# Kernel optimization log

Measured on AMD Instinct MI355X. Metric: run time of the kernel, lower is better.

Reference implementation:

```python
import jax, jax.numpy as jnp
import numpy as np

B, N, D, E, A, DIAM = 16, 1024, 128, 16384, 64, 3


def setup_inputs() -> dict:
    key = jax.random.key(0)
    ks = jax.random.split(key, 20)
    s = 0.05
    inp = {
        "node_features": jax.random.normal(ks[0], (B, N, D), jnp.float32),
        "edge_features": jax.random.normal(ks[1], (B, N, N), jnp.float32),
        "src_idx": jax.random.randint(ks[2], (E,), 0, N, jnp.int32),
        "tgt_idx": jax.random.randint(ks[3], (E,), 0, N, jnp.int32),
        # message MLP: Linear(2D+1 -> D)
        "W_msg": jax.random.normal(ks[4], (2 * D + 1, D), jnp.float32) * s,
        "b_msg": jax.random.normal(ks[5], (D,), jnp.float32) * s,
        # GRUCell(D, D), gate order r,z,n (torch convention)
        "W_ih": jax.random.normal(ks[6], (3 * D, D), jnp.float32) * s,
        "W_hh": jax.random.normal(ks[7], (3 * D, D), jnp.float32) * s,
        "b_ih": jax.random.normal(ks[8], (3 * D,), jnp.float32) * s,
        "b_hh": jax.random.normal(ks[9], (3 * D,), jnp.float32) * s,
        # readout: Linear(D,D)+SELU, Linear(D,D)+SELU, then policy head Linear(D,A)
        "W_r1": jax.random.normal(ks[10], (D, D), jnp.float32) * s,
        "b_r1": jax.random.normal(ks[11], (D,), jnp.float32) * s,
        "W_r2": jax.random.normal(ks[12], (D, D), jnp.float32) * s,
        "b_r2": jax.random.normal(ks[13], (D,), jnp.float32) * s,
        "W_pol": jax.random.normal(ks[14], (D, A), jnp.float32) * s,
        "b_pol": jax.random.normal(ks[15], (A,), jnp.float32) * s,
    }
    return inp


def reference(node_features, edge_features, src_idx, tgt_idx,
              W_msg, b_msg, W_ih, W_hh, b_ih, b_hh,
              W_r1, b_r1, W_r2, b_r2, W_pol, b_pol):
    h = node_features  # [B, N, D]
    ef = edge_features[:, src_idx, tgt_idx][..., None]  # [B, E, 1], constant across rounds
    for _ in range(DIAM):
        src_f = h[:, src_idx]  # [B, E, D] gather
        tgt_f = h[:, tgt_idx]  # [B, E, D]
        comb = jnp.concatenate([src_f, tgt_f, ef], axis=-1)  # [B, E, 2D+1]
        msg = jax.nn.selu(comb @ W_msg + b_msg)  # [B, E, D]
        # scatter-sum messages onto target nodes
        agg = jax.vmap(lambda m: jax.ops.segment_sum(m, tgt_idx, num_segments=N))(msg)  # [B, N, D]
        # GRUCell update (torch math, gate order r,z,n; b_hn stays inside r*(...))
        gi = agg @ W_ih.T + b_ih  # [B, N, 3D]
        gh = h @ W_hh.T + b_hh    # [B, N, 3D]
        i_r, i_z, i_n = jnp.split(gi, 3, axis=-1)
        h_r, h_z, h_n = jnp.split(gh, 3, axis=-1)
        r = jax.nn.sigmoid(i_r + h_r)
        z = jax.nn.sigmoid(i_z + h_z)
        n = jnp.tanh(i_n + r * h_n)
        h = (1.0 - z) * n + z * h
    pooled = h.sum(axis=1)  # [B, D]
    pooled = jax.nn.selu(pooled @ W_r1 + b_r1)
    pooled = jax.nn.selu(pooled @ W_r2 + b_r2)
    return pooled @ W_pol + b_pol  # [B, A] policy logits
```

## Files before the change

kernel.cpp:

```cpp
#include <hip/hip_runtime.h>
#include <hip/hip_bf16.h>
#include <math.h>

constexpr int kB = 16;
constexpr int kN = 1024;
constexpr int kD = 128;
constexpr int kE = 16384;

typedef short bf16x8 __attribute__((ext_vector_type(8)));
typedef float f32x4 __attribute__((ext_vector_type(4)));
typedef unsigned short us4 __attribute__((ext_vector_type(4)));

__device__ __forceinline__ float selu_f(float x) {
    const float scale = 1.0507009873554805f;
    const float alpha = 1.6732632423543772f;
    return x > 0.f ? scale * x : scale * alpha * (__expf(x) - 1.f);
}

__device__ __forceinline__ float sigmoid_f(float x) {
    return __builtin_amdgcn_rcpf(1.f + __expf(-x));
}

__device__ __forceinline__ float tanh_f(float x) {
    return 1.f - 2.f * __builtin_amdgcn_rcpf(1.f + __expf(2.f * x));
}

__device__ __forceinline__ float bf2f(unsigned short u) {
    union { unsigned int i; float f; } x;
    x.i = ((unsigned int)u) << 16;
    return x.f;
}

__device__ __forceinline__ unsigned short f2bf(float f) {
    union { float f; unsigned int i; } u;
    u.f = f;
    const unsigned int r = u.i + 0x7fffu + ((u.i >> 16) & 1u);
    return (unsigned short)(r >> 16);
}

__global__ void k_h0cw(const float* __restrict__ nodef, unsigned short* __restrict__ h_bf,
                       const int* __restrict__ tgt, int* __restrict__ cnt,
                       const float* __restrict__ Wmsg, const float* __restrict__ Whh,
                       const float* __restrict__ Wih,
                       const float* __restrict__ bih, const float* __restrict__ bhh,
                       unsigned short* __restrict__ WcatT,
                       unsigned short* __restrict__ Wfused,
                       float* __restrict__ bihP, float* __restrict__ bhhP) {
    const int bid = blockIdx.x;
    const int t = threadIdx.x;
    if (bid < 2048) {
        const int gid = bid * 256 + t;
        const float4 v = ((const float4*)nodef)[gid];
        us4 o;
        o.x = f2bf(v.x);
        o.y = f2bf(v.y);
        o.z = f2bf(v.z);
        o.w = f2bf(v.w);
        ((us4*)h_bf)[gid] = o;
        if (gid < kE) atomicAdd(&cnt[tgt[gid]], 1);
    } else {
        const int j = (bid - 2048) * 2 + (t >> 7);
        const int k = t & 127;
        if (j < 256) {
            float v = (j < 128) ? Wmsg[k * 128 + j] : Wmsg[(128 + k) * 128 + (j - 128)];
            WcatT[j * 128 + k] = f2bf(v);
        } else {
            const int f = j - 256;
            const int dg = f / 48, rem = f % 48;
            const int g = rem / 16, di = rem % 16;
            const int orig = g * 128 + dg * 16 + di;
            Wfused[(size_t)f * 256 + k] = f2bf(Wih[(size_t)orig * 128 + k]);
            Wfused[(size_t)f * 256 + 128 + k] = f2bf(Whh[(size_t)orig * 128 + k]);
            if (k == 0) {
                bihP[f] = bih[orig];
                bhhP[f] = bhh[orig];
            }
        }
    }
}

__launch_bounds__(1024)
__global__ void k_scansct(const int* __restrict__ cnt, const int* __restrict__ src,
                          const int* __restrict__ tgt, int* __restrict__ rowstart,
                          int* __restrict__ ssrc, int* __restrict__ stgt) {
    __shared__ int s[kN];
    __shared__ int cur[kN];
    const int t = threadIdx.x;
    const int own = cnt[t];
    s[t] = own;
    __syncthreads();
    for (int off = 1; off < kN; off <<= 1) {
        int add = (t >= off) ? s[t - off] : 0;
        __syncthreads();
        s[t] += add;
        __syncthreads();
    }
    const int excl = s[t] - own;
    cur[t] = excl;
    rowstart[t] = excl;
    if (t == kN - 1) rowstart[kN] = s[t];
    __syncthreads();
    for (int e = t; e < kE; e += 1024) {
        const int tg = tgt[e];
        const int pos = atomicAdd(&cur[tg], 1);
        ssrc[pos] = src[e];
        stgt[pos] = tg;
    }
}

__global__ void k_gather_ef(const float* __restrict__ edgef, const int* __restrict__ ssrc,
                            const int* __restrict__ stgt, float* __restrict__ efg) {
    const int gid = blockIdx.x * 256 + threadIdx.x;
    const int b = gid >> 14;
    const int i = gid & (kE - 1);
    efg[gid] = edgef[(size_t)b * kN * kN + (size_t)ssrc[i] * kN + stgt[i]];
}

__launch_bounds__(256)
__global__ void k_mm256(const unsigned short* __restrict__ A,
                        const unsigned short* __restrict__ Bt,
                        unsigned short* __restrict__ HST) {
    __shared__ uint4 As[2048];
    __shared__ uint4 Bs[2048];
    const int t = threadIdx.x;
    const int r0 = blockIdx.x * 128;
    const int c0 = blockIdx.y * 128;
    const uint4* gA = (const uint4*)(A + (size_t)r0 * 128);
    const uint4* gB = (const uint4*)(Bt + (size_t)c0 * 128);
#pragma unroll
    for (int i = 0; i < 8; ++i) {
        const int f = i * 256 + t;
        const int row = f >> 4, c16 = f & 15;
        const int d = row * 16 + (c16 ^ (row & 7));
        As[d] = gA[f];
        Bs[d] = gB[f];
    }
    __syncthreads();
    const int w = t >> 6, l = t & 63;
    const int wm = (w & 1) * 64, wn = (w >> 1) * 64;
    const int lin = l & 15, kq = l >> 4;
    f32x4 acc[4][4] = {};
#pragma unroll
    for (int s = 0; s < 4; ++s) {
        bf16x8 a[4], b[4];
#pragma unroll
        for (int mi = 0; mi < 4; ++mi) {
            const int row = wm + mi * 16 + lin;
            a[mi] = *(const bf16x8*)&As[row * 16 + ((s * 4 + kq) ^ (row & 7))];
        }
#pragma unroll
        for (int ni = 0; ni < 4; ++ni) {
            const int row = wn + ni * 16 + lin;
            b[ni] = *(const bf16x8*)&Bs[row * 16 + ((s * 4 + kq) ^ (row & 7))];
        }
#pragma unroll
        for (int mi = 0; mi < 4; ++mi)
#pragma unroll
            for (int ni = 0; ni < 4; ++ni)
                acc[mi][ni] = __builtin_amdgcn_mfma_f32_16x16x32_bf16(
                    b[ni], a[mi], acc[mi][ni], 0, 0, 0);
    }
    const int rq = kq * 4;
#pragma unroll
    for (int mi = 0; mi < 4; ++mi) {
        const int row = r0 + wm + mi * 16 + lin;
#pragma unroll
        for (int ni = 0; ni < 4; ++ni) {
            const int col = c0 + wn + ni * 16 + rq;
            us4 o;
            o.x = f2bf(acc[mi][ni][0]);
            o.y = f2bf(acc[mi][ni][1]);
            o.z = f2bf(acc[mi][ni][2]);
            o.w = f2bf(acc[mi][ni][3]);
            *(us4*)&HST[(size_t)row * 256 + col] = o;
        }
    }
}

__launch_bounds__(256)
__global__ void k_edge(const unsigned short* __restrict__ HST, const float* __restrict__ efg,
                       const int* __restrict__ ssrc, const int* __restrict__ rowstart,
                       const float* __restrict__ Wmsg, const float* __restrict__ bmsg,
                       unsigned short* __restrict__ agg_bf) {
    __shared__ float4 part[2][4][32];
    const int t = threadIdx.x;
    const int b = blockIdx.y;
    const int tl = t >> 7;
    const int tg = blockIdx.x * 2 + tl;
    const int slot = (t >> 5) & 3;
    const int lane = t & 31;
    const int c = lane * 4;
    const float4 w3 = *(const float4*)&Wmsg[256 * 128 + c];
    const float4 bm = *(const float4*)&bmsg[c];
    const size_t base = (size_t)b * kN;
    const us4 htu = *(const us4*)&HST[(base + tg) * 256 + 128 + c];
    const float hb0 = bf2f(htu.x) + bm.x;
    const float hb1 = bf2f(htu.y) + bm.y;
    const float hb2 = bf2f(htu.z) + bm.z;
    const float hb3 = bf2f(htu.w) + bm.w;
    const float* efb = efg + b * kE;
    const int j0 = rowstart[tg], j1 = rowstart[tg + 1];
    float a0 = 0.f, a1 = 0.f, a2 = 0.f, a3 = 0.f;
    for (int j = j0 + slot; j < j1; j += 4) {
        const int s = ssrc[j];
        const float ef = efb[j];
        const us4 hs = *(const us4*)&HST[(base + s) * 256 + c];
        a0 += selu_f(bf2f(hs.x) + fmaf(ef, w3.x, hb0));
        a1 += selu_f(bf2f(hs.y) + fmaf(ef, w3.y, hb1));
        a2 += selu_f(bf2f(hs.z) + fmaf(ef, w3.z, hb2));
        a3 += selu_f(bf2f(hs.w) + fmaf(ef, w3.w, hb3));
    }
    part[tl][slot][lane] = make_float4(a0, a1, a2, a3);
    __syncthreads();
    if (slot == 0) {
        const float4 p1 = part[tl][1][lane];
        const float4 p2 = part[tl][2][lane];
        const float4 p3 = part[tl][3][lane];
        a0 += p1.x + p2.x + p3.x;
        a1 += p1.y + p2.y + p3.y;
        a2 += p1.z + p2.z + p3.z;
        a3 += p1.w + p2.w + p3.w;
        us4 o;
        o.x = f2bf(a0);
        o.y = f2bf(a1);
        o.z = f2bf(a2);
        o.w = f2bf(a3);
        *(us4*)&agg_bf[(base + tg) * 128 + c] = o;
    }
}

__launch_bounds__(256)
__global__ void k_gigru(const unsigned short* __restrict__ agg_bf,
                        const unsigned short* __restrict__ h_bf_in,
                        const unsigned short* __restrict__ Wfused,
                        const float* __restrict__ bihP, const float* __restrict__ bhhP,
                        unsigned short* __restrict__ h_bf_out,
                        float* __restrict__ pooled, int lastIter) {
    __shared__ uint4 As[2048];
    __shared__ uint4 Bs[1536];
    const int t = threadIdx.x;
    const int r0 = blockIdx.x * 128;
    const int y = blockIdx.y;
    const int w = t >> 6, l = t & 63;
    const int wm = (w & 1) * 64, wc0 = (w >> 1) * 48;
    const int lin = l & 15, kq = l >> 4, rq = kq * 4;
    f32x4 acc[4][3] = {};
    f32x4 accN[4] = {};
#pragma unroll
    for (int stage = 0; stage < 2; ++stage) {
        const unsigned short* Ap = stage ? h_bf_in : agg_bf;
        const uint4* gA = (const uint4*)(Ap + (size_t)r0 * 128);
#pragma unroll
        for (int i = 0; i < 8; ++i) {
            const int f = i * 256 + t;
            const int row = f >> 4, c16 = f & 15;
            As[row * 16 + (c16 ^ (row & 7))] = gA[f];
        }
        const uint4* gW = (const uint4*)Wfused;
#pragma unroll
        for (int i = 0; i < 6; ++i) {
            const int f = i * 256 + t;
            const int j = f >> 4, c16 = f & 15;
            Bs[j * 16 + (c16 ^ (j & 7))] = gW[(size_t)(y * 96 + j) * 32 + stage * 16 + c16];
        }
        __syncthreads();
#pragma unroll
        for (int ks = 0; ks < 4; ++ks) {
            bf16x8 a[4], b[3];
#pragma unroll
            for (int mi = 0; mi < 4; ++mi) {
                const int row = wm + mi * 16 + lin;
                a[mi] = *(const bf16x8*)&As[row * 16 + ((ks * 4 + kq) ^ (row & 7))];
            }
#pragma unroll
            for (int ni = 0; ni < 3; ++ni) {
                const int row = wc0 + ni * 16 + lin;
                b[ni] = *(const bf16x8*)&Bs[row * 16 + ((ks * 4 + kq) ^ (row & 7))];
            }
#pragma unroll
            for (int mi = 0; mi < 4; ++mi) {
                acc[mi][0] = __builtin_amdgcn_mfma_f32_16x16x32_bf16(a[mi], b[0], acc[mi][0], 0, 0, 0);
                acc[mi][1] = __builtin_amdgcn_mfma_f32_16x16x32_bf16(a[mi], b[1], acc[mi][1], 0, 0, 0);
                if (stage == 0)
                    acc[mi][2] = __builtin_amdgcn_mfma_f32_16x16x32_bf16(a[mi], b[2], acc[mi][2], 0, 0, 0);
                else
                    accN[mi] = __builtin_amdgcn_mfma_f32_16x16x32_bf16(a[mi], b[2], accN[mi], 0, 0, 0);
            }
        }
        __syncthreads();
    }
    const int colR = y * 96 + wc0 + lin;
    const float bR = bihP[colR] + bhhP[colR];
    const float bZ = bihP[colR + 16] + bhhP[colR + 16];
    const float biN = bihP[colR + 32];
    const float bhN = bhhP[colR + 32];
    const int dgg = y * 2 + (wc0 / 48);
    const int d = dgg * 16 + lin;
    const int bb = r0 >> 10;
    const int dc = d >> 3, de = d & 7;
    float psum = 0.f;
#pragma unroll
    for (int mi = 0; mi < 4; ++mi) {
#pragma unroll
        for (int r = 0; r < 4; ++r) {
            const int rowL = wm + mi * 16 + rq + r;
            const float rr = sigmoid_f(acc[mi][0][r] + bR);
            const float zz = sigmoid_f(acc[mi][1][r] + bZ);
            const float i_n = acc[mi][2][r] + biN;
            const float h_n = accN[mi][r] + bhN;
            const float nn = tanh_f(fmaf(rr, h_n, i_n));
            const float hv = bf2f(((const unsigned short*)&As[rowL * 16 + (dc ^ (rowL & 7))])[de]);
            const float o = fmaf(zz, hv - nn, nn);
            h_bf_out[(size_t)(r0 + rowL) * 128 + d] = f2bf(o);
            psum += o;
        }
    }
    if (lastIter) atomicAdd(&pooled[bb * 128 + d], psum);
}

__global__ void k_head(const float* __restrict__ pooled,
                       const float* __restrict__ Wr1, const float* __restrict__ br1,
                       const float* __restrict__ Wr2, const float* __restrict__ br2,
                       const float* __restrict__ Wpol, const float* __restrict__ bpol,
                       float* __restrict__ out) {
    __shared__ float p[128], t1[128];
    const int b = blockIdx.x, d = threadIdx.x;
    p[d] = pooled[b * 128 + d];
    __syncthreads();
    float acc = br1[d];
    for (int k = 0; k < 128; ++k) acc = fmaf(p[k], Wr1[k * 128 + d], acc);
    t1[d] = selu_f(acc);
    __syncthreads();
    acc = br2[d];
    for (int k = 0; k < 128; ++k) acc = fmaf(t1[k], Wr2[k * 128 + d], acc);
    __syncthreads();
    p[d] = selu_f(acc);
    __syncthreads();
    if (d < 64) {
        float o = bpol[d];
        for (int k = 0; k < 128; ++k) o = fmaf(p[k], Wpol[k * 64 + d], o);
        out[b * 64 + d] = o;
    }
}

extern "C" void kernel_launch(void* const* d_in, const int* in_sizes, int n_in,
                              void* d_out, int out_size, void* d_ws, size_t ws_size,
                              hipStream_t stream) {
    const float* nodef = (const float*)d_in[0];
    const float* edgef = (const float*)d_in[1];
    const int* src = (const int*)d_in[2];
    const int* tgt = (const int*)d_in[3];
    const float* Wmsg = (const float*)d_in[4];
    const float* bmsg = (const float*)d_in[5];
    const float* Wih = (const float*)d_in[6];
    const float* Whh = (const float*)d_in[7];
    const float* bih = (const float*)d_in[8];
    const float* bhh = (const float*)d_in[9];
    const float* Wr1 = (const float*)d_in[10];
    const float* br1 = (const float*)d_in[11];
    const float* Wr2 = (const float*)d_in[12];
    const float* br2 = (const float*)d_in[13];
    const float* Wpol = (const float*)d_in[14];
    const float* bpol = (const float*)d_in[15];
    float* out = (float*)d_out;

    float* ws = (float*)d_ws;
    float* efg = ws;
    float* bihP = efg + 262144;
    float* bhhP = bihP + 384;
    int* cnt = (int*)(bhhP + 384);
    float* pooled = (float*)(cnt + 1024);
    unsigned short* HST = (unsigned short*)(pooled + 2048);
    unsigned short* hbfA = HST + 4194304;
    unsigned short* hbfB = hbfA + 2097152;
    unsigned short* agg_bf = hbfB + 2097152;
    unsigned short* WcatT = agg_bf + 2097152;
    unsigned short* Wfused = WcatT + 32768;
    int* stgt = (int*)(Wfused + 98304);
    int* rowstart = stgt + 16384;
    int* ssrc = rowstart + 1040;

    hipMemsetAsync(cnt, 0, (1024 + 2048) * sizeof(int), stream);
    k_h0cw<<<2048 + 320, 256, 0, stream>>>(nodef, hbfA, tgt, cnt, Wmsg, Whh, Wih, bih, bhh,
                                           WcatT, Wfused, bihP, bhhP);
    k_scansct<<<1, 1024, 0, stream>>>(cnt, src, tgt, rowstart, ssrc, stgt);
    k_gather_ef<<<(kB * kE) / 256, 256, 0, stream>>>(edgef, ssrc, stgt, efg);

    for (int it = 0; it < 3; ++it) {
        unsigned short* hcur = (it & 1) ? hbfB : hbfA;
        unsigned short* hnxt = (it & 1) ? hbfA : hbfB;
        k_mm256<<<dim3(128, 2), 256, 0, stream>>>(hcur, WcatT, HST);
        k_edge<<<dim3(kN / 2, kB), 256, 0, stream>>>(HST, efg, ssrc, rowstart, Wmsg, bmsg, agg_bf);
        k_gigru<<<dim3(128, 4), 256, 0, stream>>>(agg_bf, hcur, Wfused, bihP, bhhP, hnxt,
                                                  pooled, it == 2 ? 1 : 0);
    }

    k_head<<<kB, 128, 0, stream>>>(pooled, Wr1, br1, Wr2, br2, Wpol, bpol, out);
}
```

Before: 303.3 us.

## Split CSR build into wave-shuffle scan and parallel rank-based scatter

The count kernel now records each edge's atomic rank within its target bucket. The single-block scan is rewritten with wavefront shuffles instead of a barrier-heavy shared-memory Hillis-Steele scan. The scatter moves to a separate multi-block kernel that places each edge at rowstart plus its rank, removing the serial single-block atomic scatter. This adds one kernel launch and a rank buffer in the workspace, and the edge order within each bucket is now nondeterministic.

```diff
diff --git a/kernel.cpp b/kernel.cpp
--- a/kernel.cpp
+++ b/kernel.cpp
@@ -40,6 +40,7 @@
 
 __global__ void k_h0cw(const float* __restrict__ nodef, unsigned short* __restrict__ h_bf,
                        const int* __restrict__ tgt, int* __restrict__ cnt,
+                       int* __restrict__ rank,
                        const float* __restrict__ Wmsg, const float* __restrict__ Whh,
                        const float* __restrict__ Wih,
                        const float* __restrict__ bih, const float* __restrict__ bhh,
@@ -57,7 +58,7 @@
         o.z = f2bf(v.z);
         o.w = f2bf(v.w);
         ((us4*)h_bf)[gid] = o;
-        if (gid < kE) atomicAdd(&cnt[tgt[gid]], 1);
+        if (gid < kE) rank[gid] = atomicAdd(&cnt[tgt[gid]], 1);
     } else {
         const int j = (bid - 2048) * 2 + (t >> 7);
         const int k = t & 127;
@@ -80,32 +81,43 @@
 }
 
 __launch_bounds__(1024)
-__global__ void k_scansct(const int* __restrict__ cnt, const int* __restrict__ src,
-                          const int* __restrict__ tgt, int* __restrict__ rowstart,
-                          int* __restrict__ ssrc, int* __restrict__ stgt) {
-    __shared__ int s[kN];
-    __shared__ int cur[kN];
+__global__ void k_scan(const int* __restrict__ cnt, int* __restrict__ rowstart) {
+    __shared__ int wsum[16];
     const int t = threadIdx.x;
-    const int own = cnt[t];
-    s[t] = own;
-    __syncthreads();
-    for (int off = 1; off < kN; off <<= 1) {
-        int add = (t >= off) ? s[t - off] : 0;
-        __syncthreads();
-        s[t] += add;
-        __syncthreads();
-    }
-    const int excl = s[t] - own;
-    cur[t] = excl;
-    rowstart[t] = excl;
-    if (t == kN - 1) rowstart[kN] = s[t];
-    __syncthreads();
-    for (int e = t; e < kE; e += 1024) {
-        const int tg = tgt[e];
-        const int pos = atomicAdd(&cur[tg], 1);
-        ssrc[pos] = src[e];
-        stgt[pos] = tg;
-    }
+    const int lane = t & 63, wv = t >> 6;
+    const int v = cnt[t];
+    int x = v;
+#pragma unroll
+    for (int off = 1; off < 64; off <<= 1) {
+        const int y = __shfl_up(x, off, 64);
+        if (lane >= off) x += y;
+    }
+    if (lane == 63) wsum[wv] = x;
+    __syncthreads();
+    if (wv == 0 && lane < 16) {
+        const int s = wsum[lane];
+        int xs = s;
+#pragma unroll
+        for (int off = 1; off < 16; off <<= 1) {
+            const int y = __shfl_up(xs, off, 64);
+            if (lane >= off) xs += y;
+        }
+        wsum[lane] = xs - s;
+    }
+    __syncthreads();
+    const int incl = x + wsum[wv];
+    rowstart[t] = incl - v;
+    if (t == kN - 1) rowstart[kN] = incl;
+}
+
+__global__ void k_sct(const int* __restrict__ src, const int* __restrict__ tgt,
+                      const int* __restrict__ rank, const int* __restrict__ rowstart,
+                      int* __restrict__ ssrc, int* __restrict__ stgt) {
+    const int e = blockIdx.x * 256 + threadIdx.x;
+    const int tg = tgt[e];
+    const int pos = rowstart[tg] + rank[e];
+    ssrc[pos] = src[e];
+    stgt[pos] = tg;
 }
 
 __global__ void k_gather_ef(const float* __restrict__ edgef, const int* __restrict__ ssrc,
@@ -379,11 +391,13 @@
     int* stgt = (int*)(Wfused + 98304);
     int* rowstart = stgt + 16384;
     int* ssrc = rowstart + 1040;
+    int* rank = ssrc + 16384;
 
     hipMemsetAsync(cnt, 0, (1024 + 2048) * sizeof(int), stream);
-    k_h0cw<<<2048 + 320, 256, 0, stream>>>(nodef, hbfA, tgt, cnt, Wmsg, Whh, Wih, bih, bhh,
-                                           WcatT, Wfused, bihP, bhhP);
-    k_scansct<<<1, 1024, 0, stream>>>(cnt, src, tgt, rowstart, ssrc, stgt);
+    k_h0cw<<<2048 + 320, 256, 0, stream>>>(nodef, hbfA, tgt, cnt, rank, Wmsg, Whh, Wih,
+                                           bih, bhh, WcatT, Wfused, bihP, bhhP);
+    k_scan<<<1, 1024, 0, stream>>>(cnt, rowstart);
+    k_sct<<<kE / 256, 256, 0, stream>>>(src, tgt, rank, rowstart, ssrc, stgt);
     k_gather_ef<<<(kB * kE) / 256, 256, 0, stream>>>(edgef, ssrc, stgt, efg);
 
     for (int it = 0; it < 3; ++it) {
```

After: 272.6 us. -10.1%, faster.
